# Performance work log

Hardware: AMD Instinct MI355X
Metric: run time of the kernel (lower is better)

Reference implementation:

```python
import jax, jax.numpy as jnp
import numpy as np

N = 200000   # octree nodes at this depth (in_h == out_h for stride=1)
K = 27       # kdim = 3*3*3
C_IN = 32
C_OUT = 32


def setup_inputs() -> dict:
    key = jax.random.key(0)
    k1, k2, k3 = jax.random.split(key, 3)
    data = jax.random.normal(k1, (N, C_IN), dtype=jnp.float32)
    weights = jax.random.normal(k2, (K, C_IN, C_OUT), dtype=jnp.float32) * 0.05
    raw = jax.random.randint(k3, (N, K), 0, N + N // 10)
    neigh = jnp.where(raw < N, raw, -1).astype(jnp.int64)
    return {"data": data, "weights": weights, "neigh": neigh}


def reference(data, weights, neigh):
    # gather neighbor features, zero-filled where neigh == -1
    valid = neigh >= 0                                 # [N, K]
    safe_idx = jnp.where(valid, neigh, 0)
    gathered = jnp.where(valid[..., None], data[safe_idx], 0.0)  # [N, K, C_in]
    # buffered GEMM: out[n, o] = sum_{k, c} gathered[n, k, c] * weights[k, c, o]
    out = jnp.einsum('nkc,kco->no', gathered, weights)           # [N, C_out]
    return out
```

## Files before the change

### kernel.cpp

```cpp
#include <hip/hip_runtime.h>
#include <hip/hip_bf16.h>

#define N_NODES 200000
#define KDIM 27
#define C_IN 32
#define C_OUT 32

#define PF 4
#define IPD 4
#define IB (PF + IPD)

typedef __bf16 bf16x8 __attribute__((ext_vector_type(8)));
typedef float floatx4 __attribute__((ext_vector_type(4)));
typedef float float4_t __attribute__((ext_vector_type(4)));

__device__ inline bf16x8 zero_bf16x8() {
    bf16x8 z;
#pragma unroll
    for (int i = 0; i < 8; ++i) z[i] = (__bf16)0.0f;
    return z;
}

__global__ __launch_bounds__(256) void convert_data_kernel(
    const float* __restrict__ src, __bf16* __restrict__ dst) {
    int i = blockIdx.x * 256 + threadIdx.x;
    const float4_t* s = (const float4_t*)src;
    float4_t v0 = __builtin_nontemporal_load(&s[2 * i]);
    float4_t v1 = __builtin_nontemporal_load(&s[2 * i + 1]);
    bf16x8 o;
    o[0] = (__bf16)v0[0]; o[1] = (__bf16)v0[1];
    o[2] = (__bf16)v0[2]; o[3] = (__bf16)v0[3];
    o[4] = (__bf16)v1[0]; o[5] = (__bf16)v1[1];
    o[6] = (__bf16)v1[2]; o[7] = (__bf16)v1[3];
    ((bf16x8*)dst)[i] = o;
    if (blockIdx.x == 0 && threadIdx.x < 4) {
        ((bf16x8*)dst)[N_NODES * 4 + threadIdx.x] = zero_bf16x8();
    }
}

__global__ __launch_bounds__(256) void pack_weights_kernel(
    const float* __restrict__ w, __bf16* __restrict__ wp) {
    int id = blockIdx.x * 256 + threadIdx.x;
    int j = id & 7;
    int l = (id >> 3) & 63;
    int t = (id >> 9) & 1;
    int kk = id >> 10;
    int c = ((l >> 4) << 3) + j;
    int o = t * 16 + (l & 15);
    wp[id] = (__bf16)w[(kk * C_IN + c) * C_OUT + o];
}

__global__ __launch_bounds__(256, 3) void octconv_main_kernel(
    const int* __restrict__ neigh, const __bf16* __restrict__ data_bf,
    const __bf16* __restrict__ wpack, float* __restrict__ out) {
    const int tid  = threadIdx.x;
    const int wave = tid >> 6;
    const int lane = tid & 63;
    const int node_base = (blockIdx.x * 4 + wave) * 32;
    const int r16  = lane & 15;
    const int half = lane >> 4;
    const int cb   = half << 3;
    const int m0   = node_base + r16;
    const int m1   = m0 + 16;
    const int sm0 = (m0 < N_NODES) ? m0 : (N_NODES - 1);
    const int sm1 = (m1 < N_NODES) ? m1 : (N_NODES - 1);
    const int* __restrict__ nrow0 = neigh + sm0 * KDIM;
    const int* __restrict__ nrow1 = neigh + sm1 * KDIM;
    const __bf16* __restrict__ dch = data_bf + cb;
    const bf16x8* __restrict__ wp  = (const bf16x8*)wpack;

    floatx4 acc00 = {0.f, 0.f, 0.f, 0.f};
    floatx4 acc01 = {0.f, 0.f, 0.f, 0.f};
    floatx4 acc10 = {0.f, 0.f, 0.f, 0.f};
    floatx4 acc11 = {0.f, 0.f, 0.f, 0.f};

    int i0buf[IB], i1buf[IB];
    bf16x8 a0b[PF], a1b[PF], b0b[PF], b1b[PF];

#pragma unroll
    for (int t = 0; t < IB; ++t) {
        i0buf[t] = __builtin_nontemporal_load(&nrow0[t]);
        i1buf[t] = __builtin_nontemporal_load(&nrow1[t]);
    }
#pragma unroll
    for (int t = 0; t < PF; ++t) {
        unsigned u0 = (unsigned)i0buf[t]; if (u0 > (unsigned)N_NODES) u0 = N_NODES;
        unsigned u1 = (unsigned)i1buf[t]; if (u1 > (unsigned)N_NODES) u1 = N_NODES;
        a0b[t] = *(const bf16x8*)(dch + ((size_t)u0 << 5));
        a1b[t] = *(const bf16x8*)(dch + ((size_t)u1 << 5));
        b0b[t] = wp[(t * 2 + 0) * 64 + lane];
        b1b[t] = wp[(t * 2 + 1) * 64 + lane];
    }

#pragma unroll
    for (int kk = 0; kk < KDIM; ++kk) {
        const int s = kk & (PF - 1);
        acc00 = __builtin_amdgcn_mfma_f32_16x16x32_bf16(a0b[s], b0b[s], acc00, 0, 0, 0);
        acc01 = __builtin_amdgcn_mfma_f32_16x16x32_bf16(a0b[s], b1b[s], acc01, 0, 0, 0);
        acc10 = __builtin_amdgcn_mfma_f32_16x16x32_bf16(a1b[s], b0b[s], acc10, 0, 0, 0);
        acc11 = __builtin_amdgcn_mfma_f32_16x16x32_bf16(a1b[s], b1b[s], acc11, 0, 0, 0);

        if (kk + PF < KDIM) {
            const int t = kk + PF;
            unsigned u0 = (unsigned)i0buf[t & (IB - 1)]; if (u0 > (unsigned)N_NODES) u0 = N_NODES;
            unsigned u1 = (unsigned)i1buf[t & (IB - 1)]; if (u1 > (unsigned)N_NODES) u1 = N_NODES;
            a0b[s] = *(const bf16x8*)(dch + ((size_t)u0 << 5));
            a1b[s] = *(const bf16x8*)(dch + ((size_t)u1 << 5));
            b0b[s] = wp[(t * 2 + 0) * 64 + lane];
            b1b[s] = wp[(t * 2 + 1) * 64 + lane];
        }
        if (kk + IB < KDIM) {
            i0buf[kk & (IB - 1)] = __builtin_nontemporal_load(&nrow0[kk + IB]);
            i1buf[kk & (IB - 1)] = __builtin_nontemporal_load(&nrow1[kk + IB]);
        }
    }

#pragma unroll
    for (int r = 0; r < 4; ++r) {
        int row = half * 4 + r;
        int n0 = node_base + row;
        int n1 = n0 + 16;
        if (n0 < N_NODES) {
            __builtin_nontemporal_store(acc00[r], &out[n0 * C_OUT + r16]);
            __builtin_nontemporal_store(acc01[r], &out[n0 * C_OUT + 16 + r16]);
        }
        if (n1 < N_NODES) {
            __builtin_nontemporal_store(acc10[r], &out[n1 * C_OUT + r16]);
            __builtin_nontemporal_store(acc11[r], &out[n1 * C_OUT + 16 + r16]);
        }
    }
}

extern "C" void kernel_launch(void* const* d_in, const int* in_sizes, int n_in,
                              void* d_out, int out_size, void* d_ws, size_t ws_size,
                              hipStream_t stream) {
    const float* data    = (const float*)d_in[0];
    const float* weights = (const float*)d_in[1];
    const int*   neigh   = (const int*)d_in[2];
    float*       out     = (float*)d_out;

    __bf16* data_bf = (__bf16*)d_ws;
    __bf16* wpack   = (__bf16*)((char*)d_ws + (size_t)(N_NODES + 1) * C_IN * sizeof(__bf16));

    hipLaunchKernelGGL(convert_data_kernel, dim3((N_NODES * C_IN / 8 + 255) / 256),
                       dim3(256), 0, stream, data, data_bf);
    hipLaunchKernelGGL(pack_weights_kernel, dim3((KDIM * C_IN * C_OUT + 255) / 256),
                       dim3(256), 0, stream, weights, wpack);
    int blocks = (N_NODES + 127) / 128;
    hipLaunchKernelGGL(octconv_main_kernel, dim3(blocks), dim3(256), 0, stream,
                       neigh, data_bf, wpack, out);
}
```

Measured before the change: 183.5 us.

## Hand-schedule gather pipeline with inline asm loads and explicit vmcnt waits

Replaces the compiler-scheduled prefetch loop with template-unrolled stages that issue global loads via inline asm and wait with precomputed s_waitcnt vmcnt counts. Each stage waits only for the oldest outstanding fragment loads rather than letting the compiler insert conservative waits, so more gathers stay in flight across MFMA stages. The index loads are restructured so only the first four are fetched up front, and the rest are issued inside the pipeline. Hand-tuned vmcnt values are fragile: a miscount could read data before it arrives, and the sched barriers block compiler reordering.

```diff
diff --git a/kernel.cpp b/kernel.cpp
--- a/kernel.cpp
+++ b/kernel.cpp
@@ -7,8 +7,7 @@
 #define C_OUT 32
 
 #define PF 4
-#define IPD 4
-#define IB (PF + IPD)
+#define IB 8
 
 typedef __bf16 bf16x8 __attribute__((ext_vector_type(8)));
 typedef float floatx4 __attribute__((ext_vector_type(4)));
@@ -50,6 +49,80 @@
     wp[id] = (__bf16)w[(kk * C_IN + c) * C_OUT + o];
 }
 
+
+__device__ __forceinline__ void load_frag16(bf16x8& dst, const __bf16* addr) {
+    asm volatile("global_load_dwordx4 %0, %1, off" : "=v"(dst) : "v"(addr));
+}
+template<int BYTEOFF>
+__device__ __forceinline__ void load_idx(int& dst, const int* base) {
+    asm volatile("global_load_dword %0, %1, off offset:%2"
+                 : "=v"(dst) : "v"(base), "n"(BYTEOFF));
+}
+
+constexpr int wtop(int j) {
+    if (j <= 19) return 18;
+    if (j == 20) return 16;
+    if (j == 21) return 14;
+    if (j == 22 || j == 23) return 12;
+    if (j == 24) return 8;
+    if (j == 25) return 4;
+    return 0;
+}
+
+struct PipeState {
+    bf16x8 a0[PF], a1[PF], b0[PF], b1[PF];
+    int i0[IB], i1[IB];
+    floatx4 acc00, acc01, acc10, acc11;
+    const __bf16* dch;
+    const __bf16* wlane;
+    const int* nrow0;
+    const int* nrow1;
+};
+
+template<int J>
+__device__ __forceinline__ void stage(PipeState& st) {
+    asm volatile("s_waitcnt vmcnt(%0)" :: "n"(wtop(J)) : "memory");
+    __builtin_amdgcn_sched_barrier(0);
+    constexpr int s = J % PF;
+    st.acc00 = __builtin_amdgcn_mfma_f32_16x16x32_bf16(st.a0[s], st.b0[s], st.acc00, 0, 0, 0);
+    st.acc01 = __builtin_amdgcn_mfma_f32_16x16x32_bf16(st.a0[s], st.b1[s], st.acc01, 0, 0, 0);
+    st.acc10 = __builtin_amdgcn_mfma_f32_16x16x32_bf16(st.a1[s], st.b0[s], st.acc10, 0, 0, 0);
+    st.acc11 = __builtin_amdgcn_mfma_f32_16x16x32_bf16(st.a1[s], st.b1[s], st.acc11, 0, 0, 0);
+    if constexpr (J + PF < KDIM) {
+        constexpr int t = J + PF;
+        unsigned u0 = (unsigned)st.i0[t % IB]; if (u0 > (unsigned)N_NODES) u0 = N_NODES;
+        unsigned u1 = (unsigned)st.i1[t % IB]; if (u1 > (unsigned)N_NODES) u1 = N_NODES;
+        load_frag16(st.a0[s], st.dch + ((size_t)u0 << 5));
+        load_frag16(st.a1[s], st.dch + ((size_t)u1 << 5));
+        load_frag16(st.b0[s], st.wlane + t * 1024);
+        load_frag16(st.b1[s], st.wlane + t * 1024 + 512);
+        if constexpr (J + IB < KDIM) {
+            load_idx<4 * (J + IB)>(st.i0[(J + IB) % IB], st.nrow0);
+            load_idx<4 * (J + IB)>(st.i1[(J + IB) % IB], st.nrow1);
+        }
+    }
+}
+
+template<int J>
+__device__ __forceinline__ void run_stages(PipeState& st) {
+    if constexpr (J < KDIM) {
+        stage<J>(st);
+        run_stages<J + 1>(st);
+    }
+}
+
+template<int T>
+__device__ __forceinline__ void prologue_block(PipeState& st) {
+    unsigned u0 = (unsigned)st.i0[T]; if (u0 > (unsigned)N_NODES) u0 = N_NODES;
+    unsigned u1 = (unsigned)st.i1[T]; if (u1 > (unsigned)N_NODES) u1 = N_NODES;
+    load_frag16(st.a0[T], st.dch + ((size_t)u0 << 5));
+    load_frag16(st.a1[T], st.dch + ((size_t)u1 << 5));
+    load_frag16(st.b0[T], st.wlane + T * 1024);
+    load_frag16(st.b1[T], st.wlane + T * 1024 + 512);
+    load_idx<4 * (T + PF)>(st.i0[T + PF], st.nrow0);
+    load_idx<4 * (T + PF)>(st.i1[T + PF], st.nrow1);
+}
+
 __global__ __launch_bounds__(256, 3) void octconv_main_kernel(
     const int* __restrict__ neigh, const __bf16* __restrict__ data_bf,
     const __bf16* __restrict__ wpack, float* __restrict__ out) {
@@ -64,56 +137,29 @@
     const int m1   = m0 + 16;
     const int sm0 = (m0 < N_NODES) ? m0 : (N_NODES - 1);
     const int sm1 = (m1 < N_NODES) ? m1 : (N_NODES - 1);
-    const int* __restrict__ nrow0 = neigh + sm0 * KDIM;
-    const int* __restrict__ nrow1 = neigh + sm1 * KDIM;
-    const __bf16* __restrict__ dch = data_bf + cb;
-    const bf16x8* __restrict__ wp  = (const bf16x8*)wpack;
 
-    floatx4 acc00 = {0.f, 0.f, 0.f, 0.f};
-    floatx4 acc01 = {0.f, 0.f, 0.f, 0.f};
-    floatx4 acc10 = {0.f, 0.f, 0.f, 0.f};
-    floatx4 acc11 = {0.f, 0.f, 0.f, 0.f};
+    PipeState st;
+    st.dch   = data_bf + cb;
+    st.wlane = wpack + (size_t)lane * 8;
+    st.nrow0 = neigh + sm0 * KDIM;
+    st.nrow1 = neigh + sm1 * KDIM;
+    st.acc00 = floatx4{0.f, 0.f, 0.f, 0.f};
+    st.acc01 = floatx4{0.f, 0.f, 0.f, 0.f};
+    st.acc10 = floatx4{0.f, 0.f, 0.f, 0.f};
+    st.acc11 = floatx4{0.f, 0.f, 0.f, 0.f};
 
-    int i0buf[IB], i1buf[IB];
-    bf16x8 a0b[PF], a1b[PF], b0b[PF], b1b[PF];
+    load_idx<0>(st.i0[0], st.nrow0);  load_idx<0>(st.i1[0], st.nrow1);
+    load_idx<4>(st.i0[1], st.nrow0);  load_idx<4>(st.i1[1], st.nrow1);
+    load_idx<8>(st.i0[2], st.nrow0);  load_idx<8>(st.i1[2], st.nrow1);
+    load_idx<12>(st.i0[3], st.nrow0); load_idx<12>(st.i1[3], st.nrow1);
+    asm volatile("s_waitcnt vmcnt(0)" ::: "memory");
+    __builtin_amdgcn_sched_barrier(0);
+    prologue_block<0>(st);
+    prologue_block<1>(st);
+    prologue_block<2>(st);
+    prologue_block<3>(st);
 
-#pragma unroll
-    for (int t = 0; t < IB; ++t) {
-        i0buf[t] = __builtin_nontemporal_load(&nrow0[t]);
-        i1buf[t] = __builtin_nontemporal_load(&nrow1[t]);
-    }
-#pragma unroll
-    for (int t = 0; t < PF; ++t) {
-        unsigned u0 = (unsigned)i0buf[t]; if (u0 > (unsigned)N_NODES) u0 = N_NODES;
-        unsigned u1 = (unsigned)i1buf[t]; if (u1 > (unsigned)N_NODES) u1 = N_NODES;
-        a0b[t] = *(const bf16x8*)(dch + ((size_t)u0 << 5));
-        a1b[t] = *(const bf16x8*)(dch + ((size_t)u1 << 5));
-        b0b[t] = wp[(t * 2 + 0) * 64 + lane];
-        b1b[t] = wp[(t * 2 + 1) * 64 + lane];
-    }
-
-#pragma unroll
-    for (int kk = 0; kk < KDIM; ++kk) {
-        const int s = kk & (PF - 1);
-        acc00 = __builtin_amdgcn_mfma_f32_16x16x32_bf16(a0b[s], b0b[s], acc00, 0, 0, 0);
-        acc01 = __builtin_amdgcn_mfma_f32_16x16x32_bf16(a0b[s], b1b[s], acc01, 0, 0, 0);
-        acc10 = __builtin_amdgcn_mfma_f32_16x16x32_bf16(a1b[s], b0b[s], acc10, 0, 0, 0);
-        acc11 = __builtin_amdgcn_mfma_f32_16x16x32_bf16(a1b[s], b1b[s], acc11, 0, 0, 0);
-
-        if (kk + PF < KDIM) {
-            const int t = kk + PF;
-            unsigned u0 = (unsigned)i0buf[t & (IB - 1)]; if (u0 > (unsigned)N_NODES) u0 = N_NODES;
-            unsigned u1 = (unsigned)i1buf[t & (IB - 1)]; if (u1 > (unsigned)N_NODES) u1 = N_NODES;
-            a0b[s] = *(const bf16x8*)(dch + ((size_t)u0 << 5));
-            a1b[s] = *(const bf16x8*)(dch + ((size_t)u1 << 5));
-            b0b[s] = wp[(t * 2 + 0) * 64 + lane];
-            b1b[s] = wp[(t * 2 + 1) * 64 + lane];
-        }
-        if (kk + IB < KDIM) {
-            i0buf[kk & (IB - 1)] = __builtin_nontemporal_load(&nrow0[kk + IB]);
-            i1buf[kk & (IB - 1)] = __builtin_nontemporal_load(&nrow1[kk + IB]);
-        }
-    }
+    run_stages<0>(st);
 
 #pragma unroll
     for (int r = 0; r < 4; ++r) {
@@ -121,12 +167,12 @@
         int n0 = node_base + row;
         int n1 = n0 + 16;
         if (n0 < N_NODES) {
-            __builtin_nontemporal_store(acc00[r], &out[n0 * C_OUT + r16]);
-            __builtin_nontemporal_store(acc01[r], &out[n0 * C_OUT + 16 + r16]);
+            __builtin_nontemporal_store(st.acc00[r], &out[n0 * C_OUT + r16]);
+            __builtin_nontemporal_store(st.acc01[r], &out[n0 * C_OUT + 16 + r16]);
         }
         if (n1 < N_NODES) {
-            __builtin_nontemporal_store(acc10[r], &out[n1 * C_OUT + r16]);
-            __builtin_nontemporal_store(acc11[r], &out[n1 * C_OUT + 16 + r16]);
+            __builtin_nontemporal_store(st.acc10[r], &out[n1 * C_OUT + r16]);
+            __builtin_nontemporal_store(st.acc11[r], &out[n1 * C_OUT + 16 + r16]);
         }
     }
 }
```

Result: faster. 170.5 us (-7.1%).

## Partition neighbor gathers by node range, stage indices in LDS, and fuse prep kernels

Applied to the files above, without the earlier changes.

The main kernel now makes four passes over the 27 kernel offsets. Each pass gathers only neighbors inside one 50000-node range and redirects all others to the zero row, so the working set of each pass can stay in L2. The block's neighbor indices are loaded once into shared memory, and loads are issued with inline asm under hand-set vmcnt waits to keep a fixed prefetch pipeline. The conversion and weight-pack kernels are merged into one launch. In exchange, MFMA work and weight/fragment load instructions grow fourfold, with many of the extra loads hitting the zero row.

```diff
diff --git a/kernel.cpp b/kernel.cpp
--- a/kernel.cpp
+++ b/kernel.cpp
@@ -5,115 +5,150 @@
 #define KDIM 27
 #define C_IN 32
 #define C_OUT 32
-
+#define NPART 4
+#define PSIZE 50000
+#define NS (NPART * KDIM)
 #define PF 4
-#define IPD 4
-#define IB (PF + IPD)
 
 typedef __bf16 bf16x8 __attribute__((ext_vector_type(8)));
 typedef float floatx4 __attribute__((ext_vector_type(4)));
 typedef float float4_t __attribute__((ext_vector_type(4)));
 
-__device__ inline bf16x8 zero_bf16x8() {
-    bf16x8 z;
-#pragma unroll
-    for (int i = 0; i < 8; ++i) z[i] = (__bf16)0.0f;
-    return z;
+__device__ __forceinline__ void load_frag16(bf16x8& dst, const __bf16* addr) {
+    asm volatile("global_load_dwordx4 %0, %1, off" : "=v"(dst) : "v"(addr));
 }
 
-__global__ __launch_bounds__(256) void convert_data_kernel(
-    const float* __restrict__ src, __bf16* __restrict__ dst) {
-    int i = blockIdx.x * 256 + threadIdx.x;
-    const float4_t* s = (const float4_t*)src;
-    float4_t v0 = __builtin_nontemporal_load(&s[2 * i]);
-    float4_t v1 = __builtin_nontemporal_load(&s[2 * i + 1]);
-    bf16x8 o;
-    o[0] = (__bf16)v0[0]; o[1] = (__bf16)v0[1];
-    o[2] = (__bf16)v0[2]; o[3] = (__bf16)v0[3];
-    o[4] = (__bf16)v1[0]; o[5] = (__bf16)v1[1];
-    o[6] = (__bf16)v1[2]; o[7] = (__bf16)v1[3];
-    ((bf16x8*)dst)[i] = o;
-    if (blockIdx.x == 0 && threadIdx.x < 4) {
-        ((bf16x8*)dst)[N_NODES * 4 + threadIdx.x] = zero_bf16x8();
+constexpr int wt_top(int j) {
+    return (j <= NS - 4) ? 12 : (j == NS - 3 ? 8 : (j == NS - 2 ? 4 : 0));
+}
+
+__global__ __launch_bounds__(256) void prep_kernel(
+    const float* __restrict__ data, const float* __restrict__ w,
+    __bf16* __restrict__ data_bf, __bf16* __restrict__ wpack) {
+    const int b = blockIdx.x;
+    const int tid = threadIdx.x;
+    if (b < 3125) {
+        int i = b * 256 + tid;
+        const float4_t* s = (const float4_t*)data;
+        float4_t v0 = __builtin_nontemporal_load(&s[2 * i]);
+        float4_t v1 = __builtin_nontemporal_load(&s[2 * i + 1]);
+        bf16x8 o;
+        o[0] = (__bf16)v0[0]; o[1] = (__bf16)v0[1];
+        o[2] = (__bf16)v0[2]; o[3] = (__bf16)v0[3];
+        o[4] = (__bf16)v1[0]; o[5] = (__bf16)v1[1];
+        o[6] = (__bf16)v1[2]; o[7] = (__bf16)v1[3];
+        ((bf16x8*)data_bf)[i] = o;
+        if (b == 0 && tid < 4) {
+            bf16x8 z;
+#pragma unroll
+            for (int t = 0; t < 8; ++t) z[t] = (__bf16)0.0f;
+            ((bf16x8*)data_bf)[N_NODES * 4 + tid] = z;
+        }
+    } else {
+        int id = (b - 3125) * 256 + tid;
+        int j = id & 7;
+        int l = (id >> 3) & 63;
+        int t = (id >> 9) & 1;
+        int kk = id >> 10;
+        int c = ((l >> 4) << 3) + j;
+        int o = t * 16 + (l & 15);
+        wpack[id] = (__bf16)w[(kk * C_IN + c) * C_OUT + o];
     }
 }
 
-__global__ __launch_bounds__(256) void pack_weights_kernel(
-    const float* __restrict__ w, __bf16* __restrict__ wp) {
-    int id = blockIdx.x * 256 + threadIdx.x;
-    int j = id & 7;
-    int l = (id >> 3) & 63;
-    int t = (id >> 9) & 1;
-    int kk = id >> 10;
-    int c = ((l >> 4) << 3) + j;
-    int o = t * 16 + (l & 15);
-    wp[id] = (__bf16)w[(kk * C_IN + c) * C_OUT + o];
-}
+
+#define ISSUE_FRAGS(SLOT, P, KK, RAW0, RAW1)                                    \
+    {                                                                           \
+        unsigned u0_ = ((unsigned)((RAW0) - (P) * PSIZE) < (unsigned)PSIZE)     \
+                           ? (unsigned)(RAW0) : (unsigned)N_NODES;              \
+        unsigned u1_ = ((unsigned)((RAW1) - (P) * PSIZE) < (unsigned)PSIZE)     \
+                           ? (unsigned)(RAW1) : (unsigned)N_NODES;              \
+        load_frag16(a0b[SLOT], dch + ((size_t)u0_ << 5));                       \
+        load_frag16(a1b[SLOT], dch + ((size_t)u1_ << 5));                       \
+        load_frag16(b0b[SLOT], wlane + (KK) * 1024);                            \
+        load_frag16(b1b[SLOT], wlane + (KK) * 1024 + 512);                      \
+    }
+
+#define STAGE(J)                                                                \
+    {                                                                           \
+        constexpr int J_ = (J);                                                 \
+        asm volatile("s_waitcnt vmcnt(%0)" ::"n"(wt_top(J_)) : "memory");       \
+        __builtin_amdgcn_sched_barrier(0);                                      \
+        constexpr int s_ = J_ % PF;                                             \
+        acc00 = __builtin_amdgcn_mfma_f32_16x16x32_bf16(a0b[s_], b0b[s_], acc00, 0, 0, 0); \
+        acc01 = __builtin_amdgcn_mfma_f32_16x16x32_bf16(a0b[s_], b1b[s_], acc01, 0, 0, 0); \
+        acc10 = __builtin_amdgcn_mfma_f32_16x16x32_bf16(a1b[s_], b0b[s_], acc10, 0, 0, 0); \
+        acc11 = __builtin_amdgcn_mfma_f32_16x16x32_bf16(a1b[s_], b1b[s_], acc11, 0, 0, 0); \
+        if constexpr (J_ + PF < NS) {                                           \
+            constexpr int T_ = J_ + PF;                                         \
+            constexpr int P_ = T_ / KDIM;                                       \
+            constexpr int K_ = T_ % KDIM;                                       \
+            int raw0_ = rp0[J_ & 1];                                            \
+            int raw1_ = rp1[J_ & 1];                                            \
+            ISSUE_FRAGS(s_, P_, K_, raw0_, raw1_);                              \
+            if constexpr (J_ + 6 < NS) {                                        \
+                rp0[J_ & 1] = nlds[lA0 + (J_ + 6) % KDIM];                      \
+                rp1[J_ & 1] = nlds[lA1 + (J_ + 6) % KDIM];                      \
+            }                                                                   \
+        }                                                                       \
+    }
+
+#define S4(a) STAGE(a) STAGE((a) + 1) STAGE((a) + 2) STAGE((a) + 3)
 
 __global__ __launch_bounds__(256, 3) void octconv_main_kernel(
     const int* __restrict__ neigh, const __bf16* __restrict__ data_bf,
     const __bf16* __restrict__ wpack, float* __restrict__ out) {
+    __shared__ int nlds[128 * KDIM];
+
     const int tid  = threadIdx.x;
     const int wave = tid >> 6;
     const int lane = tid & 63;
-    const int node_base = (blockIdx.x * 4 + wave) * 32;
     const int r16  = lane & 15;
     const int half = lane >> 4;
     const int cb   = half << 3;
-    const int m0   = node_base + r16;
-    const int m1   = m0 + 16;
-    const int sm0 = (m0 < N_NODES) ? m0 : (N_NODES - 1);
-    const int sm1 = (m1 < N_NODES) ? m1 : (N_NODES - 1);
-    const int* __restrict__ nrow0 = neigh + sm0 * KDIM;
-    const int* __restrict__ nrow1 = neigh + sm1 * KDIM;
-    const __bf16* __restrict__ dch = data_bf + cb;
-    const bf16x8* __restrict__ wp  = (const bf16x8*)wpack;
+    const int node_base = (blockIdx.x * 4 + wave) * 32;
+
+    {
+        const long long gbase = (long long)blockIdx.x * 128 * KDIM;
+        const long long gmax  = (long long)N_NODES * KDIM;
+#pragma unroll
+        for (int t = 0; t < 14; ++t) {
+            int g = t * 256 + tid;
+            if (g < 128 * KDIM) {
+                long long gg = gbase + g;
+                nlds[g] = (gg < gmax) ? __builtin_nontemporal_load(&neigh[gg]) : -1;
+            }
+        }
+    }
+    __syncthreads();
+
+    const int lA0 = (wave * 32 + r16) * KDIM;
+    const int lA1 = lA0 + 16 * KDIM;
+    const __bf16* dch   = data_bf + cb;
+    const __bf16* wlane = wpack + (size_t)lane * 8;
 
     floatx4 acc00 = {0.f, 0.f, 0.f, 0.f};
     floatx4 acc01 = {0.f, 0.f, 0.f, 0.f};
     floatx4 acc10 = {0.f, 0.f, 0.f, 0.f};
     floatx4 acc11 = {0.f, 0.f, 0.f, 0.f};
 
-    int i0buf[IB], i1buf[IB];
     bf16x8 a0b[PF], a1b[PF], b0b[PF], b1b[PF];
+    int rp0[2], rp1[2];
 
-#pragma unroll
-    for (int t = 0; t < IB; ++t) {
-        i0buf[t] = __builtin_nontemporal_load(&nrow0[t]);
-        i1buf[t] = __builtin_nontemporal_load(&nrow1[t]);
+    {
+        int q0, q1;
+        q0 = nlds[lA0 + 0]; q1 = nlds[lA1 + 0]; ISSUE_FRAGS(0, 0, 0, q0, q1);
+        q0 = nlds[lA0 + 1]; q1 = nlds[lA1 + 1]; ISSUE_FRAGS(1, 0, 1, q0, q1);
+        q0 = nlds[lA0 + 2]; q1 = nlds[lA1 + 2]; ISSUE_FRAGS(2, 0, 2, q0, q1);
+        q0 = nlds[lA0 + 3]; q1 = nlds[lA1 + 3]; ISSUE_FRAGS(3, 0, 3, q0, q1);
     }
-#pragma unroll
-    for (int t = 0; t < PF; ++t) {
-        unsigned u0 = (unsigned)i0buf[t]; if (u0 > (unsigned)N_NODES) u0 = N_NODES;
-        unsigned u1 = (unsigned)i1buf[t]; if (u1 > (unsigned)N_NODES) u1 = N_NODES;
-        a0b[t] = *(const bf16x8*)(dch + ((size_t)u0 << 5));
-        a1b[t] = *(const bf16x8*)(dch + ((size_t)u1 << 5));
-        b0b[t] = wp[(t * 2 + 0) * 64 + lane];
-        b1b[t] = wp[(t * 2 + 1) * 64 + lane];
-    }
+    rp0[0] = nlds[lA0 + 4]; rp1[0] = nlds[lA1 + 4];
+    rp0[1] = nlds[lA0 + 5]; rp1[1] = nlds[lA1 + 5];
 
-#pragma unroll
-    for (int kk = 0; kk < KDIM; ++kk) {
-        const int s = kk & (PF - 1);
-        acc00 = __builtin_amdgcn_mfma_f32_16x16x32_bf16(a0b[s], b0b[s], acc00, 0, 0, 0);
-        acc01 = __builtin_amdgcn_mfma_f32_16x16x32_bf16(a0b[s], b1b[s], acc01, 0, 0, 0);
-        acc10 = __builtin_amdgcn_mfma_f32_16x16x32_bf16(a1b[s], b0b[s], acc10, 0, 0, 0);
-        acc11 = __builtin_amdgcn_mfma_f32_16x16x32_bf16(a1b[s], b1b[s], acc11, 0, 0, 0);
-
-        if (kk + PF < KDIM) {
-            const int t = kk + PF;
-            unsigned u0 = (unsigned)i0buf[t & (IB - 1)]; if (u0 > (unsigned)N_NODES) u0 = N_NODES;
-            unsigned u1 = (unsigned)i1buf[t & (IB - 1)]; if (u1 > (unsigned)N_NODES) u1 = N_NODES;
-            a0b[s] = *(const bf16x8*)(dch + ((size_t)u0 << 5));
-            a1b[s] = *(const bf16x8*)(dch + ((size_t)u1 << 5));
-            b0b[s] = wp[(t * 2 + 0) * 64 + lane];
-            b1b[s] = wp[(t * 2 + 1) * 64 + lane];
-        }
-        if (kk + IB < KDIM) {
-            i0buf[kk & (IB - 1)] = __builtin_nontemporal_load(&nrow0[kk + IB]);
-            i1buf[kk & (IB - 1)] = __builtin_nontemporal_load(&nrow1[kk + IB]);
-        }
-    }
+    S4(0)   S4(4)   S4(8)   S4(12)  S4(16)  S4(20)  S4(24)
+    S4(28)  S4(32)  S4(36)  S4(40)  S4(44)  S4(48)  S4(52)
+    S4(56)  S4(60)  S4(64)  S4(68)  S4(72)  S4(76)  S4(80)
+    S4(84)  S4(88)  S4(92)  S4(96)  S4(100) S4(104)
 
 #pragma unroll
     for (int r = 0; r < 4; ++r) {
@@ -142,10 +177,8 @@
     __bf16* data_bf = (__bf16*)d_ws;
     __bf16* wpack   = (__bf16*)((char*)d_ws + (size_t)(N_NODES + 1) * C_IN * sizeof(__bf16));
 
-    hipLaunchKernelGGL(convert_data_kernel, dim3((N_NODES * C_IN / 8 + 255) / 256),
-                       dim3(256), 0, stream, data, data_bf);
-    hipLaunchKernelGGL(pack_weights_kernel, dim3((KDIM * C_IN * C_OUT + 255) / 256),
-                       dim3(256), 0, stream, weights, wpack);
+    hipLaunchKernelGGL(prep_kernel, dim3(3125 + 108), dim3(256), 0, stream,
+                       data, weights, data_bf, wpack);
     int blocks = (N_NODES + 127) / 128;
     hipLaunchKernelGGL(octconv_main_kernel, dim3(blocks), dim3(256), 0, stream,
                        neigh, data_bf, wpack, out);
```

New measurement: 262.6 us. 43.1% more time.
